# Kernel optimization log

Measured on AMD Instinct MI355X. Metric: run time of the kernel, lower is better.

## Reference

```python
import jax, jax.numpy as jnp
import numpy as np

EMBED = 1024
HEADS = 16
HEAD_DIM = EMBED // HEADS
MLP_HIDDEN = 4096


def _layernorm(x, g, b, eps=1e-5):
    mu = jnp.mean(x, axis=-1, keepdims=True)
    var = jnp.mean(jnp.square(x - mu), axis=-1, keepdims=True)
    return (x - mu) * jax.lax.rsqrt(var + eps) * g + b


def setup_inputs() -> dict:
    key = jax.random.key(0)
    ks = jax.random.split(key, 8)
    s = 0.02
    return {
        "x": jax.random.normal(ks[0], (8, 1024, EMBED), dtype=jnp.float32),
        "qkv_w": jax.random.normal(ks[1], (EMBED, 3 * EMBED), dtype=jnp.float32) * s,
        "qkv_b": jnp.zeros((3 * EMBED,), jnp.float32),
        "proj_w": jax.random.normal(ks[2], (EMBED, EMBED), dtype=jnp.float32) * s,
        "proj_b": jnp.zeros((EMBED,), jnp.float32),
        "fc1_w": jax.random.normal(ks[3], (EMBED, MLP_HIDDEN), dtype=jnp.float32) * s,
        "fc1_b": jnp.zeros((MLP_HIDDEN,), jnp.float32),
        "fc2_w": jax.random.normal(ks[4], (MLP_HIDDEN, EMBED), dtype=jnp.float32) * s,
        "fc2_b": jnp.zeros((EMBED,), jnp.float32),
        "ln1_g": jnp.ones((EMBED,), jnp.float32),
        "ln1_b": jnp.zeros((EMBED,), jnp.float32),
        "ln2_g": jnp.ones((EMBED,), jnp.float32),
        "ln2_b": jnp.zeros((EMBED,), jnp.float32),
    }


def reference(x, qkv_w, qkv_b, proj_w, proj_b, fc1_w, fc1_b, fc2_w, fc2_b,
              ln1_g, ln1_b, ln2_g, ln2_b):
    B, N, C = x.shape
    scale = HEAD_DIM ** -0.5

    # --- MHSA on pre-norm input ---
    h = _layernorm(x, ln1_g, ln1_b)
    qkv = h @ qkv_w + qkv_b                      # [B,N,3C]
    qkv = qkv.reshape(B, N, 3, HEADS, HEAD_DIM)
    q, k, v = (qkv[:, :, i].transpose(0, 2, 1, 3) for i in range(3))  # [B,H,N,d]
    attn = jnp.einsum('bhqd,bhkd->bhqk', q, k) * scale
    attn = jax.nn.softmax(attn, axis=-1)
    o = jnp.einsum('bhqk,bhkd->bhqd', attn, v)   # [B,H,N,d]
    o = o.transpose(0, 2, 1, 3).reshape(B, N, C)
    x = x + (o @ proj_w + proj_b)

    # --- MLP ---
    h2 = _layernorm(x, ln2_g, ln2_b)
    h2 = jax.nn.gelu(h2 @ fc1_w + fc1_b, approximate=False)
    x = x + (h2 @ fc2_w + fc2_b)
    return x
```

## Files before the change

kernel.cpp:

```cpp
#include <hip/hip_runtime.h>
#include <hip/hip_bf16.h>

typedef __bf16 bf16x8 __attribute__((ext_vector_type(8)));
typedef float  f32x4  __attribute__((ext_vector_type(4)));
typedef unsigned short u16;

static __device__ __forceinline__ u16 f2bf(float f) {
  union { float f; unsigned u; } v; v.f = f;
  unsigned r = v.u + 0x7fffu + ((v.u >> 16) & 1u);
  return (u16)(r >> 16);
}

static __device__ __forceinline__ void gld16(const void* g, void* l) {
  __builtin_amdgcn_global_load_lds(
      (const __attribute__((address_space(1))) unsigned int*)g,
      (__attribute__((address_space(3))) unsigned int*)l, 16, 0, 0);
}

#define SBAR() do { __builtin_amdgcn_sched_barrier(0); \
                    __builtin_amdgcn_s_barrier(); \
                    __builtin_amdgcn_sched_barrier(0); } while (0)

__global__ __launch_bounds__(256) void transpose_cast_k(
    const float* __restrict__ W, u16* __restrict__ Wt, int K, int N) {
  __shared__ float tile[32][33];
  const int t = threadIdx.x;
  const int n0 = blockIdx.x * 32, k0 = blockIdx.y * 32;
  const int r = t >> 3, c4 = (t & 7) * 4;
  const float4 v = *(const float4*)(W + (size_t)(k0 + r) * N + n0 + c4);
  tile[r][c4 + 0] = v.x; tile[r][c4 + 1] = v.y;
  tile[r][c4 + 2] = v.z; tile[r][c4 + 3] = v.w;
  __syncthreads();
  const int n = t >> 3, k4 = (t & 7) * 4;
  uint2 pk;
  pk.x = f2bf(tile[k4 + 0][n]) | ((unsigned)f2bf(tile[k4 + 1][n]) << 16);
  pk.y = f2bf(tile[k4 + 2][n]) | ((unsigned)f2bf(tile[k4 + 3][n]) << 16);
  *(uint2*)(Wt + (size_t)(n0 + n) * K + k0 + k4) = pk;
}

__global__ __launch_bounds__(256) void ln_cast_k(
    const float* __restrict__ x, const float* __restrict__ g,
    const float* __restrict__ b, u16* __restrict__ out) {
  __shared__ float red[2][4];
  const int t = threadIdx.x;
  const size_t row = blockIdx.x;
  const float4 v = *(const float4*)(x + row * 1024 + t * 4);
  float s = v.x + v.y + v.z + v.w;
  float ss = v.x * v.x + v.y * v.y + v.z * v.z + v.w * v.w;
  #pragma unroll
  for (int m = 1; m <= 32; m <<= 1) { s += __shfl_xor(s, m); ss += __shfl_xor(ss, m); }
  if ((t & 63) == 0) { red[0][t >> 6] = s; red[1][t >> 6] = ss; }
  __syncthreads();
  s  = red[0][0] + red[0][1] + red[0][2] + red[0][3];
  ss = red[1][0] + red[1][1] + red[1][2] + red[1][3];
  const float mu = s * (1.f / 1024.f);
  const float var = ss * (1.f / 1024.f) - mu * mu;
  const float rs = rsqrtf(var + 1e-5f);
  const float4 gv = *(const float4*)(g + t * 4);
  const float4 bv = *(const float4*)(b + t * 4);
  uint2 pk;
  pk.x = f2bf((v.x - mu) * rs * gv.x + bv.x) |
         ((unsigned)f2bf((v.y - mu) * rs * gv.y + bv.y) << 16);
  pk.y = f2bf((v.z - mu) * rs * gv.z + bv.z) |
         ((unsigned)f2bf((v.w - mu) * rs * gv.w + bv.w) << 16);
  *(uint2*)(out + row * 1024 + t * 4) = pk;
}

template <int EPI, int WN>
__global__ __launch_bounds__(512, 2) void gemm8_k(
    const u16* __restrict__ A, const u16* __restrict__ Bt,
    const float* __restrict__ bias, u16* __restrict__ Cb, float* __restrict__ Cf,
    const float* __restrict__ R, u16* __restrict__ vT, int M, int N, int K) {
  constexpr int MR = 2 * WN;
  constexpr int BN = 64 * WN;
  __shared__ u16 As[2][16384];
  __shared__ u16 Bs[2][WN * 4096];
  const int t = threadIdx.x;
  const int nt = N / BN;
  const int q = gridDim.x >> 3;
  const int swz = (blockIdx.x & 7) * q + (blockIdx.x >> 3);
  const int tn = swz % nt, tm = swz / nt;
  const int lo = t & 15, hi = (t >> 4) & 3, wid = t >> 6;
  const int wm = wid / WN, wn = wid & (WN - 1);
  const int NT = K >> 6;

  const int srow = t >> 3;
  const int sc = (t & 7) ^ (srow & 7);
  const u16* gA = A  + (size_t)(tm * 256) * K;
  const u16* gB = Bt + (size_t)(tn * BN) * K;
  auto stA = [&](int dd, int c, int T) {
    gld16(gA + (size_t)(c * 64 + srow) * K + (size_t)T * 64 + sc * 8,
          &As[dd][c * 4096 + t * 8]);
  };
  auto stB = [&](int dd, int c, int T) {
    gld16(gB + (size_t)(c * 64 + srow) * K + (size_t)T * 64 + sc * 8,
          &Bs[dd][c * 4096 + t * 8]);
  };

  const int xr = lo & 7;
  const int rowA = wm * (MR * 16) + lo;
  const int rowB = wn * 64 + lo;
#define RD_A(d, m, kk) (*(const bf16x8*)&As[d][(rowA + (m)*16)*64 + ((((kk)<<2)+hi)^xr)*8])
#define RD_B(d, n, kk) (*(const bf16x8*)&Bs[d][(rowB + (n)*16)*64 + ((((kk)<<2)+hi)^xr)*8])
#define MF(a, b, c) __builtin_amdgcn_mfma_f32_16x16x32_bf16(a, b, c, 0, 0, 0)

  f32x4 acc[MR][4];
  #pragma unroll
  for (int i = 0; i < MR; ++i)
    #pragma unroll
    for (int j = 0; j < 4; ++j) acc[i][j] = (f32x4){0.f, 0.f, 0.f, 0.f};

#define PH16(d, M0, M1, STAGES, WAITS) do { \
    bf16x8 a0 = RD_A(d, M0, 0), a1 = RD_A(d, M0, 1); \
    bf16x8 a2 = RD_A(d, M1, 0), a3 = RD_A(d, M1, 1); \
    STAGES; SBAR(); __builtin_amdgcn_s_setprio(1); \
    acc[M0][0]=MF(a0,b00,acc[M0][0]); acc[M0][1]=MF(a0,b10,acc[M0][1]); \
    acc[M0][2]=MF(a0,b20,acc[M0][2]); acc[M0][3]=MF(a0,b30,acc[M0][3]); \
    acc[M1][0]=MF(a2,b00,acc[M1][0]); acc[M1][1]=MF(a2,b10,acc[M1][1]); \
    acc[M1][2]=MF(a2,b20,acc[M1][2]); acc[M1][3]=MF(a2,b30,acc[M1][3]); \
    acc[M0][0]=MF(a1,b01,acc[M0][0]); acc[M0][1]=MF(a1,b11,acc[M0][1]); \
    acc[M0][2]=MF(a1,b21,acc[M0][2]); acc[M0][3]=MF(a1,b31,acc[M0][3]); \
    acc[M1][0]=MF(a3,b01,acc[M1][0]); acc[M1][1]=MF(a3,b11,acc[M1][1]); \
    acc[M1][2]=MF(a3,b21,acc[M1][2]); acc[M1][3]=MF(a3,b31,acc[M1][3]); \
    __builtin_amdgcn_s_setprio(0); WAITS; SBAR(); } while (0)

#define PH8(d, M0, STAGES, WAITS) do { \
    bf16x8 a0 = RD_A(d, M0, 0), a1 = RD_A(d, M0, 1); \
    STAGES; SBAR(); __builtin_amdgcn_s_setprio(1); \
    acc[M0][0]=MF(a0,b00,acc[M0][0]); acc[M0][1]=MF(a0,b10,acc[M0][1]); \
    acc[M0][2]=MF(a0,b20,acc[M0][2]); acc[M0][3]=MF(a0,b30,acc[M0][3]); \
    acc[M0][0]=MF(a1,b01,acc[M0][0]); acc[M0][1]=MF(a1,b11,acc[M0][1]); \
    acc[M0][2]=MF(a1,b21,acc[M0][2]); acc[M0][3]=MF(a1,b31,acc[M0][3]); \
    __builtin_amdgcn_s_setprio(0); WAITS; SBAR(); } while (0)

  if constexpr (WN == 4) {
    stA(0, 0, 0); stA(0, 1, 0); stA(0, 2, 0); stA(0, 3, 0);
    stB(0, 0, 0); stB(0, 1, 0); stB(0, 2, 0); stB(0, 3, 0);
    stB(1, 0, 1); stB(1, 1, 1); stB(1, 2, 1); stB(1, 3, 1);
    stA(1, 0, 1); stA(1, 2, 1);
    asm volatile("s_waitcnt vmcnt(6)" ::: "memory");
    SBAR();
    for (int T = 0; T < NT; ++T) {
      const int d = T & 1, dn = d ^ 1;
      bf16x8 b00 = RD_B(d,0,0), b01 = RD_B(d,0,1), b10 = RD_B(d,1,0), b11 = RD_B(d,1,1);
      bf16x8 b20 = RD_B(d,2,0), b21 = RD_B(d,2,1), b30 = RD_B(d,3,0), b31 = RD_B(d,3,1);
      PH16(d, 0, 1, { if (T + 1 < NT) { stA(dn, 1, T + 1); stA(dn, 3, T + 1); } }, );
      PH16(d, 2, 3, { if (T + 2 < NT) { stB(d, 0, T + 2); stB(d, 1, T + 2); } }, );
      PH16(d, 4, 5, { if (T + 2 < NT) { stB(d, 2, T + 2); stB(d, 3, T + 2); } }, );
      PH16(d, 6, 7, { if (T + 2 < NT) { stA(d, 0, T + 2); stA(d, 2, T + 2); } },
           { if (T < NT - 2)       { asm volatile("s_waitcnt vmcnt(6)" ::: "memory"); }
             else if (T == NT - 2) { asm volatile("s_waitcnt vmcnt(0)" ::: "memory"); } });
    }
  } else {
    stA(0, 0, 0); stA(0, 1, 0); stA(0, 2, 0); stA(0, 3, 0);
    stB(0, 0, 0); stB(0, 1, 0);
    stB(1, 0, 1); stB(1, 1, 1);
    asm volatile("s_waitcnt vmcnt(2)" ::: "memory");
    SBAR();
    for (int T = 0; T < NT; ++T) {
      const int d = T & 1, dn = d ^ 1;
      bf16x8 b00 = RD_B(d,0,0), b01 = RD_B(d,0,1), b10 = RD_B(d,1,0), b11 = RD_B(d,1,1);
      bf16x8 b20 = RD_B(d,2,0), b21 = RD_B(d,2,1), b30 = RD_B(d,3,0), b31 = RD_B(d,3,1);
      PH8(d, 0, { if (T + 1 < NT) { stA(dn, 0, T + 1); stA(dn, 1, T + 1);
                                    stA(dn, 2, T + 1); stA(dn, 3, T + 1); } }, );
      PH8(d, 1, { if (T + 2 < NT) { stB(d, 0, T + 2); stB(d, 1, T + 2); } }, );
      PH8(d, 2, , );
      PH8(d, 3, ,
          { if (T < NT - 2)       { asm volatile("s_waitcnt vmcnt(2)" ::: "memory"); }
            else if (T == NT - 2) { asm volatile("s_waitcnt vmcnt(0)" ::: "memory"); } });
    }
  }

  #pragma unroll
  for (int ni = 0; ni < 4; ++ni) {
    const int col = tn * BN + wn * 64 + ni * 16 + lo;
    const float bv = bias[col];
    #pragma unroll
    for (int mi = 0; mi < MR; ++mi) {
      const int row0 = tm * 256 + wm * (MR * 16) + mi * 16 + hi * 4;
      const f32x4 v = acc[mi][ni];
      float vals[4];
      #pragma unroll
      for (int r = 0; r < 4; ++r) {
        float val = v[r] + bv;
        if (EPI == 1) val = 0.5f * val * (1.f + erff(val * 0.70710678118f));
        vals[r] = val;
      }
      if (EPI == 2) {
        #pragma unroll
        for (int r = 0; r < 4; ++r) {
          const size_t idx = (size_t)(row0 + r) * N + col;
          Cf[idx] = vals[r] + R[idx];
        }
      } else {
        #pragma unroll
        for (int r = 0; r < 4; ++r)
          Cb[(size_t)(row0 + r) * N + col] = f2bf(vals[r]);
        if (EPI == 3 && col >= 2048) {
          const int bb = row0 >> 10, n = row0 & 1023;
          const int hh = (col - 2048) >> 6, dd = col & 63;
          uint2 pk;
          pk.x = f2bf(vals[0]) | ((unsigned)f2bf(vals[1]) << 16);
          pk.y = f2bf(vals[2]) | ((unsigned)f2bf(vals[3]) << 16);
          *(uint2*)(vT + ((size_t)((bb * 16 + hh) * 64 + dd) << 10) + n) = pk;
        }
      }
    }
  }
#undef RD_A
#undef RD_B
#undef MF
#undef PH16
#undef PH8
}

__global__ __launch_bounds__(256, 2) void attn_k(
    const u16* __restrict__ qkv, const u16* __restrict__ vT, u16* __restrict__ o) {
  __shared__ u16 lK[64 * 64];
  __shared__ u16 lV[64 * 64];
  __shared__ u16 lP[64 * 72];
  const int t = threadIdx.x;
  const int lo = t & 15, hi = (t >> 4) & 3, w = t >> 6;
  const int qt = blockIdx.x & 15, bh = blockIdx.x >> 4;
  const int b = bh >> 4, h = bh & 15;
  const int q0 = qt * 64;
  const u16* Qb = qkv + (size_t)b * 1024 * 3072 + h * 64;
  const u16* Kb = Qb + 1024;
  const u16* Vt = vT + (size_t)bh * 64 * 1024;

  bf16x8 qf[2];
  {
    const size_t q = q0 + w * 16 + lo;
    qf[0] = *(const bf16x8*)(Qb + q * 3072 + hi * 8);
    qf[1] = *(const bf16x8*)(Qb + q * 3072 + 32 + hi * 8);
  }
  f32x4 oacc[4];
  #pragma unroll
  for (int i = 0; i < 4; ++i) oacc[i] = (f32x4){0.f, 0.f, 0.f, 0.f};
  float m = -1e30f, lsum = 0.f;
  const int srow = t >> 3, scol = (t & 7) * 8;

  for (int kv0 = 0; kv0 < 1024; kv0 += 64) {
    __syncthreads();
    #pragma unroll
    for (int j = 0; j < 2; ++j) {
      const int row = j * 32 + srow;
      gld16(Kb + (size_t)(kv0 + row) * 3072 + scol, &lK[(j * 256 + t) * 8]);
      gld16(Vt + (size_t)row * 1024 + kv0 + scol, &lV[(j * 256 + t) * 8]);
    }
    __syncthreads();

    f32x4 s[4];
    #pragma unroll
    for (int i = 0; i < 4; ++i) s[i] = (f32x4){0.f, 0.f, 0.f, 0.f};
    #pragma unroll
    for (int kk = 0; kk < 2; ++kk) {
      #pragma unroll
      for (int mi = 0; mi < 4; ++mi) {
        const bf16x8 kf = *(const bf16x8*)&lK[(mi * 16 + lo) * 64 + kk * 32 + hi * 8];
        s[mi] = __builtin_amdgcn_mfma_f32_16x16x32_bf16(kf, qf[kk], s[mi], 0, 0, 0);
      }
    }
    float sv[16];
    float tmax = -1e30f;
    #pragma unroll
    for (int mi = 0; mi < 4; ++mi)
      #pragma unroll
      for (int r = 0; r < 4; ++r) {
        const float xx = s[mi][r] * 0.125f;
        sv[mi * 4 + r] = xx;
        tmax = fmaxf(tmax, xx);
      }
    tmax = fmaxf(tmax, __shfl_xor(tmax, 16));
    tmax = fmaxf(tmax, __shfl_xor(tmax, 32));
    const float mnew = fmaxf(m, tmax);
    const float alpha = __expf(m - mnew);
    m = mnew;
    float p[16], ts = 0.f;
    #pragma unroll
    for (int i = 0; i < 16; ++i) { p[i] = __expf(sv[i] - mnew); ts += p[i]; }
    ts += __shfl_xor(ts, 16);
    ts += __shfl_xor(ts, 32);
    lsum = lsum * alpha + ts;
    #pragma unroll
    for (int mi = 0; mi < 4; ++mi) {
      uint2 pk;
      pk.x = f2bf(p[mi * 4 + 0]) | ((unsigned)f2bf(p[mi * 4 + 1]) << 16);
      pk.y = f2bf(p[mi * 4 + 2]) | ((unsigned)f2bf(p[mi * 4 + 3]) << 16);
      *(uint2*)&lP[(w * 16 + lo) * 72 + mi * 16 + hi * 4] = pk;
    }
    asm volatile("s_waitcnt lgkmcnt(0)" ::: "memory");
    float ar[4];
    #pragma unroll
    for (int r = 0; r < 4; ++r) ar[r] = __shfl(alpha, hi * 4 + r);
    #pragma unroll
    for (int ni = 0; ni < 4; ++ni)
      #pragma unroll
      for (int r = 0; r < 4; ++r) oacc[ni][r] *= ar[r];
    #pragma unroll
    for (int kk = 0; kk < 2; ++kk) {
      const bf16x8 pf = *(const bf16x8*)&lP[(w * 16 + lo) * 72 + kk * 32 + hi * 8];
      #pragma unroll
      for (int ni = 0; ni < 4; ++ni) {
        const bf16x8 vf = *(const bf16x8*)&lV[(ni * 16 + lo) * 64 + kk * 32 + hi * 8];
        oacc[ni] = __builtin_amdgcn_mfma_f32_16x16x32_bf16(pf, vf, oacc[ni], 0, 0, 0);
      }
    }
  }
  float lr[4];
  #pragma unroll
  for (int r = 0; r < 4; ++r) lr[r] = 1.f / __shfl(lsum, hi * 4 + r);
  #pragma unroll
  for (int ni = 0; ni < 4; ++ni) {
    const int d = ni * 16 + lo;
    #pragma unroll
    for (int r = 0; r < 4; ++r) {
      const int n = q0 + w * 16 + hi * 4 + r;
      o[((size_t)(b * 1024 + n) * 16 + h) * 64 + d] = f2bf(oacc[ni][r] * lr[r]);
    }
  }
}

extern "C" void kernel_launch(void* const* d_in, const int* in_sizes, int n_in,
                              void* d_out, int out_size, void* d_ws, size_t ws_size,
                              hipStream_t stream) {
  const float* x      = (const float*)d_in[0];
  const float* qkv_w  = (const float*)d_in[1];
  const float* qkv_b  = (const float*)d_in[2];
  const float* proj_w = (const float*)d_in[3];
  const float* proj_b = (const float*)d_in[4];
  const float* fc1_w  = (const float*)d_in[5];
  const float* fc1_b  = (const float*)d_in[6];
  const float* fc2_w  = (const float*)d_in[7];
  const float* fc2_b  = (const float*)d_in[8];
  const float* ln1_g  = (const float*)d_in[9];
  const float* ln1_b  = (const float*)d_in[10];
  const float* ln2_g  = (const float*)d_in[11];
  const float* ln2_b  = (const float*)d_in[12];
  float* out = (float*)d_out;
  char* ws = (char*)d_ws;
  u16* wqkvT = (u16*)(ws);
  u16* wprojT = (u16*)(ws + 6291456);
  u16* wfc1T = (u16*)(ws + 8388608);
  u16* wfc2T = (u16*)(ws + 16777216);
  u16* hbuf  = (u16*)(ws + 25165824);
  u16* qkvo  = (u16*)(ws + 41943040);
  u16* vT    = (u16*)(ws + 92274688);
  u16* fc1o  = qkvo;

  transpose_cast_k<<<dim3(96, 32),  256, 0, stream>>>(qkv_w,  wqkvT, 1024, 3072);
  transpose_cast_k<<<dim3(32, 32),  256, 0, stream>>>(proj_w, wprojT, 1024, 1024);
  transpose_cast_k<<<dim3(128, 32), 256, 0, stream>>>(fc1_w,  wfc1T, 1024, 4096);
  transpose_cast_k<<<dim3(32, 128), 256, 0, stream>>>(fc2_w,  wfc2T, 4096, 1024);
  ln_cast_k<<<8192, 256, 0, stream>>>(x, ln1_g, ln1_b, hbuf);
  gemm8_k<3, 2><<<768, 512, 0, stream>>>(hbuf, wqkvT, qkv_b, qkvo, nullptr, nullptr, vT, 8192, 3072, 1024);
  attn_k<<<2048, 256, 0, stream>>>(qkvo, vT, hbuf);
  gemm8_k<2, 2><<<256, 512, 0, stream>>>(hbuf, wprojT, proj_b, nullptr, out, x, nullptr, 8192, 1024, 1024);
  ln_cast_k<<<8192, 256, 0, stream>>>(out, ln2_g, ln2_b, hbuf);
  gemm8_k<1, 4><<<512, 512, 0, stream>>>(hbuf, wfc1T, fc1_b, fc1o, nullptr, nullptr, nullptr, 8192, 4096, 1024);
  gemm8_k<2, 2><<<256, 512, 0, stream>>>(fc1o, wfc2T, fc2_b, nullptr, out, out, nullptr, 8192, 1024, 4096);
}
```

Measured before the change: 427.2 us.

## Stage GEMM bf16 epilogue through LDS for coalesced stores and cheaper GELU

Merges the A/B shared buffers into one array and reuses it after the main loop to stage the bf16 output tile, then writes it with 16-byte coalesced stores. The V-transpose output for the QKV GEMM is also gathered from LDS and written as contiguous 8-element vectors instead of scattered 8-byte stores. The QKV GEMM switches to the wider 256-column tile so a block covers whole V column ranges. GELU is replaced by an exp-based tanh approximation, trading exactness against erf for fewer instructions.

```diff
diff --git a/kernel.cpp b/kernel.cpp
--- a/kernel.cpp
+++ b/kernel.cpp
@@ -73,8 +73,8 @@
     const float* __restrict__ R, u16* __restrict__ vT, int M, int N, int K) {
   constexpr int MR = 2 * WN;
   constexpr int BN = 64 * WN;
-  __shared__ u16 As[2][16384];
-  __shared__ u16 Bs[2][WN * 4096];
+  constexpr int SHSZ = 32768 + WN * 8192;
+  __shared__ u16 SH[SHSZ];
   const int t = threadIdx.x;
   const int nt = N / BN;
   const int q = gridDim.x >> 3;
@@ -90,18 +90,18 @@
   const u16* gB = Bt + (size_t)(tn * BN) * K;
   auto stA = [&](int dd, int c, int T) {
     gld16(gA + (size_t)(c * 64 + srow) * K + (size_t)T * 64 + sc * 8,
-          &As[dd][c * 4096 + t * 8]);
+          &SH[dd * 16384 + c * 4096 + t * 8]);
   };
   auto stB = [&](int dd, int c, int T) {
     gld16(gB + (size_t)(c * 64 + srow) * K + (size_t)T * 64 + sc * 8,
-          &Bs[dd][c * 4096 + t * 8]);
+          &SH[32768 + dd * (WN * 4096) + c * 4096 + t * 8]);
   };
 
   const int xr = lo & 7;
   const int rowA = wm * (MR * 16) + lo;
   const int rowB = wn * 64 + lo;
-#define RD_A(d, m, kk) (*(const bf16x8*)&As[d][(rowA + (m)*16)*64 + ((((kk)<<2)+hi)^xr)*8])
-#define RD_B(d, n, kk) (*(const bf16x8*)&Bs[d][(rowB + (n)*16)*64 + ((((kk)<<2)+hi)^xr)*8])
+#define RD_A(d, m, kk) (*(const bf16x8*)&SH[(d)*16384 + (rowA + (m)*16)*64 + ((((kk)<<2)+hi)^xr)*8])
+#define RD_B(d, n, kk) (*(const bf16x8*)&SH[32768 + (d)*(WN*4096) + (rowB + (n)*16)*64 + ((((kk)<<2)+hi)^xr)*8])
 #define MF(a, b, c) __builtin_amdgcn_mfma_f32_16x16x32_bf16(a, b, c, 0, 0, 0)
 
   f32x4 acc[MR][4];
@@ -171,38 +171,72 @@
     }
   }
 
-  #pragma unroll
-  for (int ni = 0; ni < 4; ++ni) {
-    const int col = tn * BN + wn * 64 + ni * 16 + lo;
-    const float bv = bias[col];
-    #pragma unroll
-    for (int mi = 0; mi < MR; ++mi) {
-      const int row0 = tm * 256 + wm * (MR * 16) + mi * 16 + hi * 4;
-      const f32x4 v = acc[mi][ni];
-      float vals[4];
-      #pragma unroll
-      for (int r = 0; r < 4; ++r) {
-        float val = v[r] + bv;
-        if (EPI == 1) val = 0.5f * val * (1.f + erff(val * 0.70710678118f));
-        vals[r] = val;
-      }
-      if (EPI == 2) {
+  if constexpr (EPI == 2) {
+    #pragma unroll
+    for (int ni = 0; ni < 4; ++ni) {
+      const int col = tn * BN + wn * 64 + ni * 16 + lo;
+      const float bv = bias[col];
+      #pragma unroll
+      for (int mi = 0; mi < MR; ++mi) {
+        const int row0 = tm * 256 + wm * (MR * 16) + mi * 16 + hi * 4;
         #pragma unroll
         for (int r = 0; r < 4; ++r) {
           const size_t idx = (size_t)(row0 + r) * N + col;
-          Cf[idx] = vals[r] + R[idx];
+          Cf[idx] = acc[mi][ni][r] + bv + R[idx];
         }
-      } else {
+      }
+    }
+  } else {
+    #pragma unroll
+    for (int ni = 0; ni < 4; ++ni) {
+      const int colL = wn * 64 + ni * 16 + lo;
+      const float bv = bias[tn * BN + colL];
+      #pragma unroll
+      for (int mi = 0; mi < MR; ++mi) {
+        const int rowL = wm * (MR * 16) + mi * 16 + hi * 4;
         #pragma unroll
-        for (int r = 0; r < 4; ++r)
-          Cb[(size_t)(row0 + r) * N + col] = f2bf(vals[r]);
-        if (EPI == 3 && col >= 2048) {
-          const int bb = row0 >> 10, n = row0 & 1023;
-          const int hh = (col - 2048) >> 6, dd = col & 63;
-          uint2 pk;
-          pk.x = f2bf(vals[0]) | ((unsigned)f2bf(vals[1]) << 16);
-          pk.y = f2bf(vals[2]) | ((unsigned)f2bf(vals[3]) << 16);
-          *(uint2*)(vT + ((size_t)((bb * 16 + hh) * 64 + dd) << 10) + n) = pk;
+        for (int r = 0; r < 4; ++r) {
+          float val = acc[mi][ni][r] + bv;
+          if (EPI == 1) {
+            const float u = 0.79788456f * val * (1.f + 0.044715f * val * val);
+            const float e = __expf(fminf(2.f * u, 80.f));
+            val = val * (e / (e + 1.f));
+          }
+          SH[(rowL + r) * BN + colL] = f2bf(val);
+        }
+      }
+    }
+    __syncthreads();
+    constexpr int ROWSH = (BN == 256) ? 9 : 8;
+    const int base = t * 16;
+    #pragma unroll
+    for (int p = 0; p < BN / 16; ++p) {
+      const int o = base + p * 8192;
+      const int row = o >> ROWSH;
+      const int cb = (o & (2 * BN - 1)) >> 1;
+      const uint4 v4 = *(const uint4*)&SH[o >> 1];
+      *(uint4*)(Cb + (size_t)(tm * 256 + row) * N + tn * BN + cb) = v4;
+    }
+    if constexpr (EPI == 3) {
+      if (tn >= 8) {
+        const int c = t & 255;
+        const int rg = t >> 8;
+        const int gcol = tn * 256 + c;
+        const int hh = (gcol - 2048) >> 6, dd = gcol & 63;
+        const int bb = tm >> 2, nb = (tm & 3) * 256;
+        u16* dst = vT + ((size_t)((bb * 16 + hh) * 64 + dd) << 10) + nb + rg * 128;
+        #pragma unroll
+        for (int i = 0; i < 16; ++i) {
+          const int r0 = rg * 128 + i * 8;
+          u16 tv[8];
+          #pragma unroll
+          for (int j = 0; j < 8; ++j) tv[j] = SH[(r0 + j) * 256 + c];
+          uint4 pk;
+          pk.x = tv[0] | ((unsigned)tv[1] << 16);
+          pk.y = tv[2] | ((unsigned)tv[3] << 16);
+          pk.z = tv[4] | ((unsigned)tv[5] << 16);
+          pk.w = tv[6] | ((unsigned)tv[7] << 16);
+          *(uint4*)(dst + i * 8) = pk;
         }
       }
     }
@@ -353,7 +387,7 @@
   transpose_cast_k<<<dim3(128, 32), 256, 0, stream>>>(fc1_w,  wfc1T, 1024, 4096);
   transpose_cast_k<<<dim3(32, 128), 256, 0, stream>>>(fc2_w,  wfc2T, 4096, 1024);
   ln_cast_k<<<8192, 256, 0, stream>>>(x, ln1_g, ln1_b, hbuf);
-  gemm8_k<3, 2><<<768, 512, 0, stream>>>(hbuf, wqkvT, qkv_b, qkvo, nullptr, nullptr, vT, 8192, 3072, 1024);
+  gemm8_k<3, 4><<<384, 512, 0, stream>>>(hbuf, wqkvT, qkv_b, qkvo, nullptr, nullptr, vT, 8192, 3072, 1024);
   attn_k<<<2048, 256, 0, stream>>>(qkvo, vT, hbuf);
   gemm8_k<2, 2><<<256, 512, 0, stream>>>(hbuf, wprojT, proj_b, nullptr, out, x, nullptr, 8192, 1024, 1024);
   ln_cast_k<<<8192, 256, 0, stream>>>(out, ln2_g, ln2_b, hbuf);
```

Result: faster. 403.0 us (-5.7%).
